# Kernel optimization log

Hardware: AMD Instinct MI355X
Metric: run time of the kernel (lower is better)

The kernel has to match this reference:

```python
import jax, jax.numpy as jnp
import numpy as np

B, N, DIN, DOUT = 8, 2048, 256, 256

def setup_inputs() -> dict:
    key = jax.random.key(0)
    k1, k2, k3 = jax.random.split(key, 3)
    H = jax.random.normal(k1, (B, N, DIN), dtype=jnp.float32)
    G = jax.random.uniform(k2, (B, N, N), dtype=jnp.float32)  # positive -> nonzero row/col sums
    # xavier_uniform-style scale for the weight
    limit = float(np.sqrt(6.0 / (DIN + DOUT)))
    W = jax.random.uniform(k3, (DIN, DOUT), dtype=jnp.float32, minval=-limit, maxval=limit)
    return {"H": H, "G": G, "W": W}

def reference(H, G, W):
    # N_e = H @ W : [b,n,dout]
    N_e = H @ W
    # symmetric part
    G_F = (G + jnp.swapaxes(G, 1, 2)) * 0.5
    # loop over k of outer products == two normalized Gram matrices:
    # G_Sin[i,j] = sum_k G[k,i]*G[k,j] / rowsum_k  == G^T diag(1/rowsum) G
    # G_So[i,j]  = sum_k G[i,k]*G[j,k] / colsum_k  == G diag(1/colsum) G^T
    rs = G.sum(axis=-1)  # [b,n] row sums
    cs = G.sum(axis=-2)  # [b,n] col sums
    G_Sin = jnp.einsum('bki,bkj->bij', G / rs[:, :, None], G)
    G_So = jnp.einsum('bik,bjk->bij', G / cs[:, None, :], G)
    H_out = jnp.concatenate([
        jax.nn.relu(G_F @ N_e),
        jax.nn.relu(G_Sin @ N_e),
        jax.nn.relu(G_So @ N_e),
    ], axis=-1)  # [b,n,3*dout]
    return H_out
```

## Files before the change

### kernel.cpp

```cpp
#include <hip/hip_runtime.h>
#include <hip/hip_bf16.h>


constexpr int NN = 2048;
constexpr long GSTR = (long)NN * NN;

using frag8   = __attribute__((ext_vector_type(8))) short;
using floatx4 = __attribute__((ext_vector_type(4))) float;
using ush8    = __attribute__((ext_vector_type(8))) unsigned short;

__device__ inline unsigned short f2bf(float x) {
    unsigned u = __float_as_uint(x);
    u += 0x7FFF + ((u >> 16) & 1);
    return (unsigned short)(u >> 16);
}
__device__ inline float bf2f(unsigned short h) {
    return __uint_as_float((unsigned)h << 16);
}
__device__ inline ushort2 pk2(float a, float b) {
    union { __hip_bfloat162 h; ushort2 u; } cv;
    cv.h = __float22bfloat162_rn(float2{a, b});
    return cv.u;
}
__device__ inline void gload_lds16(const void* g, void* l) {
    __builtin_amdgcn_global_load_lds(
        (const __attribute__((address_space(1))) void*)g,
        (__attribute__((address_space(3))) void*)l, 16, 0, 0);
}

enum { EPI_NE = 0, EPI_M1 = 1, EPI_P2 = 2, EPI_O3 = 3 };
enum { A_F32ROW = 0, A_DMA = 1 };

template <int EPI, int AMODE, int TM, int NJ>
__global__ __launch_bounds__(256) void mgemm(
    const void* __restrict__ Aptr,
    const unsigned short* __restrict__ B0,
    const unsigned short* __restrict__ B1,
    const float* __restrict__ rsraw,
    unsigned short* __restrict__ CsT,
    float* __restrict__ outp,
    const float* __restrict__ scale,
    int K, int lda, long strideA, long sB)
{
    constexpr int MF = TM / 32;
    __shared__ __align__(16) unsigned short As[TM * 64];
    __shared__ __align__(16) unsigned short Bs[64 * 64];

    const int t  = threadIdx.x;
    const int bx = blockIdx.x;
    const int xcd = bx & 7;
    const int kk  = bx >> 3;
    constexpr int PER = NJ * 8;
    const int itile = xcd + 8 * (kk / PER);
    const int rem   = kk & (PER - 1);
    const int bb    = rem / NJ;
    const int jt    = rem & (NJ - 1);
    const int i0b = itile * TM;
    const int j0  = jt * 64;

    const unsigned short* Btb =
        ((EPI == EPI_P2 && j0 >= 256) ? B1 + (long)(j0 - 256) * K
                                      : B0 + (long)j0 * K) + (long)bb * sB;

    const int w = t >> 6, l = t & 63;
    const int wm = w >> 1, wn = w & 1;
    const int quad = l >> 4, c15 = l & 15;

    const int lr  = l >> 3, ls = l & 7;

    floatx4 acc[MF][2] = {};

    for (int k0 = 0; k0 < K; k0 += 64) {
        if constexpr (AMODE == A_DMA) {
            const unsigned short* Au = (const unsigned short*)Aptr
                + (long)bb * strideA
                + (((long)itile * (K >> 7) + (k0 >> 7)) << 14);
            const int kin = k0 & 127;
            #pragma unroll
            for (int q = 0; q < TM / 32; ++q) {
                const int rt = q * 32 + w * 8;
                gload_lds16(Au + (rt + lr) * 128 + kin + ((ls ^ lr) << 3),
                            &As[rt * 64]);
            }
        } else {
            const float* Af = (const float*)Aptr + (long)bb * strideA;
            const int ar  = t >> 2;
            const int ac0 = (t & 3) * 2;
            const float* ap = Af + (long)(i0b + ar) * lda + k0 + ac0 * 8;
            const float4 x0 = *(const float4*)(ap + 0);
            const float4 x1 = *(const float4*)(ap + 4);
            const float4 x2 = *(const float4*)(ap + 8);
            const float4 x3 = *(const float4*)(ap + 12);
            union { ush8 v; ushort2 u2[4]; } p0, p1;
            p0.u2[0] = pk2(x0.x, x0.y); p0.u2[1] = pk2(x0.z, x0.w);
            p0.u2[2] = pk2(x1.x, x1.y); p0.u2[3] = pk2(x1.z, x1.w);
            p1.u2[0] = pk2(x2.x, x2.y); p1.u2[1] = pk2(x2.z, x2.w);
            p1.u2[2] = pk2(x3.x, x3.y); p1.u2[3] = pk2(x3.z, x3.w);
            const int sw = ar & 7;
            *(ush8*)&As[ar * 64 + ((ac0 ^ sw) << 3)]       = p0.v;
            *(ush8*)&As[ar * 64 + (((ac0 + 1) ^ sw) << 3)] = p1.v;
        }
        #pragma unroll
        for (int q = 0; q < 2; ++q) {
            const int rt = w * 16 + q * 8;
            gload_lds16(Btb + (long)(rt + lr) * K + k0 + ((ls ^ lr) << 3),
                        &Bs[rt * 64]);
        }
        __syncthreads();

        #pragma unroll
        for (int ks = 0; ks < 2; ++ks) {
            frag8 af[MF], bfv[2];
            const int swr = c15 & 7;
            #pragma unroll
            for (int mt = 0; mt < MF; ++mt)
                af[mt] = *(const frag8*)&As[(wm * (TM / 2) + mt * 16 + c15) * 64
                                            + (((ks * 4 + quad) ^ swr) << 3)];
            #pragma unroll
            for (int nt = 0; nt < 2; ++nt)
                bfv[nt] = *(const frag8*)&Bs[(wn * 32 + nt * 16 + c15) * 64
                                             + (((ks * 4 + quad) ^ swr) << 3)];
            #pragma unroll
            for (int mt = 0; mt < MF; ++mt)
                #pragma unroll
                for (int nt = 0; nt < 2; ++nt)
                    acc[mt][nt] = __builtin_amdgcn_mfma_f32_16x16x32_bf16(
                        af[mt], bfv[nt], acc[mt][nt], 0, 0, 0);
        }
        __syncthreads();
    }

    const long rowb = (long)bb * NN;
    #pragma unroll
    for (int mt = 0; mt < MF; ++mt) {
        const int il = wm * (TM / 2) + mt * 16 + quad * 4;
        const int ib = i0b + il;
        float4 s4 = make_float4(1.f, 1.f, 1.f, 1.f);
        if constexpr (EPI == EPI_M1) s4 = *(const float4*)(scale + rowb + ib);
        if constexpr (EPI == EPI_P2) {
            if (j0 < 256) s4 = *(const float4*)(scale + rowb + ib);
        }
        #pragma unroll
        for (int nt = 0; nt < 2; ++nt) {
            floatx4 v = acc[mt][nt];
            const int gj = j0 + wn * 32 + nt * 16 + c15;
            if constexpr (EPI == EPI_NE) {
                union { ushort4 v; ushort2 u2[2]; } p;
                p.u2[0] = pk2(v[0], v[1]); p.u2[1] = pk2(v[2], v[3]);
                *(ushort4*)(CsT + ((long)bb * 256 + gj) * 2048 + ib) = p.v;
            } else if constexpr (EPI == EPI_M1) {
                union { ushort4 v; ushort2 u2[2]; } p;
                p.u2[0] = pk2(v[0] * s4.x, v[1] * s4.y);
                p.u2[1] = pk2(v[2] * s4.z, v[3] * s4.w);
                *(ushort4*)(CsT + ((long)bb * 256 + gj) * 2048 + ib) = p.v;
            } else if constexpr (EPI == EPI_P2) {
                if (j0 < 256) {
                    union { ushort4 v; ushort2 u2[2]; } p;
                    p.u2[0] = pk2(v[0] * s4.x, v[1] * s4.y);
                    p.u2[1] = pk2(v[2] * s4.z, v[3] * s4.w);
                    *(ushort4*)(CsT + ((long)bb * 256 + gj) * 2048 + ib) = p.v;
                    const float4 rr = *(const float4*)(rsraw + rowb + ib);
                    const ushort4 m1p = *(const ushort4*)(B1 + ((long)bb * 256 + gj) * 2048 + ib);
                    const float m1v[4] = {bf2f(m1p.x) * rr.x, bf2f(m1p.y) * rr.y,
                                          bf2f(m1p.z) * rr.z, bf2f(m1p.w) * rr.w};
                    #pragma unroll
                    for (int r = 0; r < 4; ++r)
                        outp[(rowb + ib + r) * 768 + gj] = fmaxf(0.5f * (v[r] + m1v[r]), 0.f);
                } else {
                    #pragma unroll
                    for (int r = 0; r < 4; ++r)
                        outp[(rowb + ib + r) * 768 + gj] = fmaxf(v[r], 0.f);
                }
            } else {
                #pragma unroll
                for (int r = 0; r < 4; ++r)
                    outp[(rowb + ib + r) * 768 + 512 + gj] = fmaxf(v[r], 0.f);
            }
        }
    }
}

__global__ __launch_bounds__(256) void cvt_g(
    const float* __restrict__ G,
    unsigned short* __restrict__ Gbf, unsigned short* __restrict__ GbfT,
    float* __restrict__ prs, float* __restrict__ pcs)
{
    const int b  = blockIdx.z;
    const int j0 = blockIdx.x * 128, i0 = blockIdx.y * 128;
    const int t  = threadIdx.x;
    const int w  = t >> 6, l = t & 63;
    const int wm = w >> 1, wn = w & 1;
    const int rg = l >> 3, c = l & 7;

    const int ib = i0 + wm * 64 + rg * 8;
    const int jb = j0 + wn * 64 + c * 8;
    const int il = wm * 64 + rg * 8;
    const int jl = wn * 64 + c * 8;

    const long gbase = (long)b * GSTR + (((long)blockIdx.y * 16 + blockIdx.x) << 14);
    const long tbase = (long)b * GSTR + (((long)blockIdx.x * 16 + blockIdx.y) << 14);

    const float* gp = G + (long)b * GSTR + (long)ib * NN + jb;

    float4 xs[16];
    #pragma unroll
    for (int r = 0; r < 8; ++r) {
        xs[2 * r]     = *(const float4*)(gp + (long)r * NN);
        xs[2 * r + 1] = *(const float4*)(gp + (long)r * NN + 4);
    }
    __builtin_amdgcn_sched_barrier(0);

    union RowU { ush8 v; ushort2 u2[4]; unsigned u4[4]; };
    RowU rows[8];
    float csum[8] = {};
    float rsum[8];

    #pragma unroll
    for (int r = 0; r < 8; ++r) {
        const float4 x0 = xs[2 * r], x1 = xs[2 * r + 1];
        RowU rw;
        rw.u2[0] = pk2(x0.x, x0.y); rw.u2[1] = pk2(x0.z, x0.w);
        rw.u2[2] = pk2(x1.x, x1.y); rw.u2[3] = pk2(x1.z, x1.w);
        rows[r] = rw;
        *(ush8*)(Gbf + gbase + (long)(il + r) * 128 + jl) = rw.v;
        rsum[r] = x0.x + x0.y + x0.z + x0.w + x1.x + x1.y + x1.z + x1.w;
        csum[0] += x0.x; csum[1] += x0.y; csum[2] += x0.z; csum[3] += x0.w;
        csum[4] += x1.x; csum[5] += x1.y; csum[6] += x1.z; csum[7] += x1.w;
    }

    #pragma unroll
    for (int r = 0; r < 8; ++r) {
        rsum[r] += __shfl_xor(rsum[r], 1);
        rsum[r] += __shfl_xor(rsum[r], 2);
        rsum[r] += __shfl_xor(rsum[r], 4);
    }
    if (c == 0) {
        float* pp = prs + ((long)b * 32 + blockIdx.x * 2 + wn) * NN + ib;
        *(float4*)pp       = make_float4(rsum[0], rsum[1], rsum[2], rsum[3]);
        *(float4*)(pp + 4) = make_float4(rsum[4], rsum[5], rsum[6], rsum[7]);
    }

    #pragma unroll
    for (int e = 0; e < 8; ++e) {
        csum[e] += __shfl_xor(csum[e], 8);
        csum[e] += __shfl_xor(csum[e], 16);
        csum[e] += __shfl_xor(csum[e], 32);
    }
    if (rg == 0) {
        float* pp = pcs + ((long)b * 32 + blockIdx.y * 2 + wm) * NN + jb;
        *(float4*)pp       = make_float4(csum[0], csum[1], csum[2], csum[3]);
        *(float4*)(pp + 4) = make_float4(csum[4], csum[5], csum[6], csum[7]);
    }

    RowU cols[8];
    #pragma unroll
    for (int p = 0; p < 4; ++p) {
        #pragma unroll
        for (int k = 0; k < 4; ++k) {
            const unsigned a = rows[2 * p].u4[k], bq = rows[2 * p + 1].u4[k];
            cols[2 * k].u4[p]     = (a & 0xffffu) | (bq << 16);
            cols[2 * k + 1].u4[p] = (a >> 16) | (bq & 0xffff0000u);
        }
    }
    #pragma unroll
    for (int j = 0; j < 8; ++j)
        *(ush8*)(GbfT + tbase + (long)(jl + j) * 128 + il) = cols[j].v;
}

__global__ __launch_bounds__(256) void finalize(
    const float* __restrict__ prs, const float* __restrict__ pcs,
    float* __restrict__ inv_rs, float* __restrict__ rs_raw,
    float* __restrict__ inv_cs,
    const float* __restrict__ W, unsigned short* __restrict__ Wt)
{
    const int idx = blockIdx.x * 256 + threadIdx.x;
    if (blockIdx.y == 0) {
        const int b = idx >> 11, i = idx & 2047;
        float s = 0.f;
        #pragma unroll
        for (int jc = 0; jc < 32; ++jc) s += prs[((long)b * 32 + jc) * NN + i];
        inv_rs[idx] = 1.0f / s;
        rs_raw[idx] = s;
    } else if (blockIdx.y == 1) {
        const int b = idx >> 11, i = idx & 2047;
        float s = 0.f;
        #pragma unroll
        for (int ic = 0; ic < 32; ++ic) s += pcs[((long)b * 32 + ic) * NN + i];
        inv_cs[idx] = 1.0f / s;
    } else {
        #pragma unroll
        for (int e = 0; e < 4; ++e) {
            const int flat = idx * 4 + e;
            const int j = flat >> 8, k = flat & 255;
            Wt[flat] = f2bf(W[(long)k * 256 + j]);
        }
    }
}

extern "C" void kernel_launch(void* const* d_in, const int* in_sizes, int n_in,
                              void* d_out, int out_size, void* d_ws, size_t ws_size,
                              hipStream_t stream)
{
    constexpr int B = 8;
    const float* H = (const float*)d_in[0];
    const float* G = (const float*)d_in[1];
    const float* W = (const float*)d_in[2];
    float* out = (float*)d_out;

    unsigned short* ws16 = (unsigned short*)d_ws;
    unsigned short* Gbf  = ws16;
    unsigned short* GbfT = Gbf  + (long)B * GSTR;
    unsigned short* Wt   = GbfT + (long)B * GSTR;
    unsigned short* NeT  = Wt   + 65536;
    unsigned short* M1sT = NeT  + 4194304;
    unsigned short* M2sT = M1sT + 4194304;
    float* inv_rs = (float*)(M2sT + 4194304);
    float* rs_raw = inv_rs + 16384;
    float* inv_cs = rs_raw + 16384;
    float* prs    = inv_cs + 16384;
    float* pcs    = prs + (long)B * 32 * NN;

    cvt_g<<<dim3(16, 16, 8), 256, 0, stream>>>(G, Gbf, GbfT, prs, pcs);
    finalize<<<dim3(64, 3), 256, 0, stream>>>(prs, pcs, inv_rs, rs_raw, inv_cs, W, Wt);

    const long sNT = 256L * NN;
    mgemm<EPI_NE, A_F32ROW, 64, 4><<<1024, 256, 0, stream>>>(
        H, Wt, nullptr, nullptr, NeT, nullptr, nullptr,
        256, 256, 2048L * 256, 0);
    mgemm<EPI_M1, A_DMA, 128, 4><<<512, 256, 0, stream>>>(
        Gbf, NeT, nullptr, nullptr, M1sT, nullptr, inv_rs,
        2048, 2048, GSTR, sNT);
    mgemm<EPI_P2, A_DMA, 128, 8><<<1024, 256, 0, stream>>>(
        GbfT, NeT, M1sT, rs_raw, M2sT, out, inv_cs,
        2048, 2048, GSTR, sNT);
    mgemm<EPI_O3, A_DMA, 128, 4><<<512, 256, 0, stream>>>(
        Gbf, M2sT, nullptr, nullptr, nullptr, out, nullptr,
        2048, 2048, GSTR, sNT);
}
```

Baseline: 392.8 us.

## Split G conversion into streaming pass plus bf16 transpose; widen P2 N-tile

The fused fp32 G conversion/transpose kernel is split in two. A row-streaming kernel converts G to tiled bf16, computes full row sums directly and writes column partials. A second kernel then builds the transposed bf16 copy by reading the bf16 tiles rather than fp32. The mgemm template gains a WJ tile-width parameter, and the P2 GEMM uses 128-wide N tiles with half the blocks, which raises A-tile reuse and register pressure. The transpose now re-reads bf16 data in an extra launch, and the finalize step sums 128 column partials instead of 32.

```diff
diff --git a/kernel.cpp b/kernel.cpp
--- a/kernel.cpp
+++ b/kernel.cpp
@@ -31,7 +31,7 @@
 enum { EPI_NE = 0, EPI_M1 = 1, EPI_P2 = 2, EPI_O3 = 3 };
 enum { A_F32ROW = 0, A_DMA = 1 };
 
-template <int EPI, int AMODE, int TM, int NJ>
+template <int EPI, int AMODE, int TM, int WJ, int NJ>
 __global__ __launch_bounds__(256) void mgemm(
     const void* __restrict__ Aptr,
     const unsigned short* __restrict__ B0,
@@ -43,8 +43,9 @@
     int K, int lda, long strideA, long sB)
 {
     constexpr int MF = TM / 32;
+    constexpr int NF = WJ / 32;
     __shared__ __align__(16) unsigned short As[TM * 64];
-    __shared__ __align__(16) unsigned short Bs[64 * 64];
+    __shared__ __align__(16) unsigned short Bs[WJ * 64];
 
     const int t  = threadIdx.x;
     const int bx = blockIdx.x;
@@ -56,7 +57,7 @@
     const int bb    = rem / NJ;
     const int jt    = rem & (NJ - 1);
     const int i0b = itile * TM;
-    const int j0  = jt * 64;
+    const int j0  = jt * WJ;
 
     const unsigned short* Btb =
         ((EPI == EPI_P2 && j0 >= 256) ? B1 + (long)(j0 - 256) * K
@@ -68,7 +69,7 @@
 
     const int lr  = l >> 3, ls = l & 7;
 
-    floatx4 acc[MF][2] = {};
+    floatx4 acc[MF][NF] = {};
 
     for (int k0 = 0; k0 < K; k0 += 64) {
         if constexpr (AMODE == A_DMA) {
@@ -101,8 +102,8 @@
             *(ush8*)&As[ar * 64 + (((ac0 + 1) ^ sw) << 3)] = p1.v;
         }
         #pragma unroll
-        for (int q = 0; q < 2; ++q) {
-            const int rt = w * 16 + q * 8;
+        for (int q = 0; q < WJ / 32; ++q) {
+            const int rt = q * 32 + w * 8;
             gload_lds16(Btb + (long)(rt + lr) * K + k0 + ((ls ^ lr) << 3),
                         &Bs[rt * 64]);
         }
@@ -110,20 +111,20 @@
 
         #pragma unroll
         for (int ks = 0; ks < 2; ++ks) {
-            frag8 af[MF], bfv[2];
+            frag8 af[MF], bfv[NF];
             const int swr = c15 & 7;
             #pragma unroll
             for (int mt = 0; mt < MF; ++mt)
                 af[mt] = *(const frag8*)&As[(wm * (TM / 2) + mt * 16 + c15) * 64
                                             + (((ks * 4 + quad) ^ swr) << 3)];
             #pragma unroll
-            for (int nt = 0; nt < 2; ++nt)
-                bfv[nt] = *(const frag8*)&Bs[(wn * 32 + nt * 16 + c15) * 64
+            for (int nt = 0; nt < NF; ++nt)
+                bfv[nt] = *(const frag8*)&Bs[(wn * (WJ / 2) + nt * 16 + c15) * 64
                                              + (((ks * 4 + quad) ^ swr) << 3)];
             #pragma unroll
             for (int mt = 0; mt < MF; ++mt)
                 #pragma unroll
-                for (int nt = 0; nt < 2; ++nt)
+                for (int nt = 0; nt < NF; ++nt)
                     acc[mt][nt] = __builtin_amdgcn_mfma_f32_16x16x32_bf16(
                         af[mt], bfv[nt], acc[mt][nt], 0, 0, 0);
         }
@@ -141,9 +142,9 @@
             if (j0 < 256) s4 = *(const float4*)(scale + rowb + ib);
         }
         #pragma unroll
-        for (int nt = 0; nt < 2; ++nt) {
+        for (int nt = 0; nt < NF; ++nt) {
             floatx4 v = acc[mt][nt];
-            const int gj = j0 + wn * 32 + nt * 16 + c15;
+            const int gj = j0 + wn * (WJ / 2) + nt * 16 + c15;
             if constexpr (EPI == EPI_NE) {
                 union { ushort4 v; ushort2 u2[2]; } p;
                 p.u2[0] = pk2(v[0], v[1]); p.u2[1] = pk2(v[2], v[3]);
@@ -180,79 +181,87 @@
     }
 }
 
-__global__ __launch_bounds__(256) void cvt_g(
+__global__ __launch_bounds__(256) void cvt_stream(
     const float* __restrict__ G,
-    unsigned short* __restrict__ Gbf, unsigned short* __restrict__ GbfT,
-    float* __restrict__ prs, float* __restrict__ pcs)
+    unsigned short* __restrict__ Gbf,
+    float* __restrict__ pcs,
+    float* __restrict__ inv_rs, float* __restrict__ rs_raw)
+{
+    __shared__ float sm[4][16];
+    const int b  = blockIdx.y;
+    const int s  = blockIdx.x;
+    const int i0 = s * 16;
+    const int t  = threadIdx.x;
+    const int c8 = t * 8;
+    const int w  = t >> 6, l = t & 63;
+
+    const float* gp = G + (long)b * GSTR + (long)i0 * NN + c8;
+    unsigned short* gb = Gbf + (long)b * GSTR;
+    const int tc = c8 >> 7, cin = c8 & 127;
+
+    float csum[8] = {};
+    float rp[16];
+
+    #pragma unroll
+    for (int r = 0; r < 16; ++r) {
+        const float4 x0 = *(const float4*)(gp + (long)r * NN);
+        const float4 x1 = *(const float4*)(gp + (long)r * NN + 4);
+        union { ush8 v; ushort2 u2[4]; } pk;
+        pk.u2[0] = pk2(x0.x, x0.y); pk.u2[1] = pk2(x0.z, x0.w);
+        pk.u2[2] = pk2(x1.x, x1.y); pk.u2[3] = pk2(x1.z, x1.w);
+        const int gi = i0 + r;
+        *(ush8*)(gb + (((long)(gi >> 7) * 16 + tc) << 14) + ((gi & 127) << 7) + cin) = pk.v;
+        rp[r] = x0.x + x0.y + x0.z + x0.w + x1.x + x1.y + x1.z + x1.w;
+        csum[0] += x0.x; csum[1] += x0.y; csum[2] += x0.z; csum[3] += x0.w;
+        csum[4] += x1.x; csum[5] += x1.y; csum[6] += x1.z; csum[7] += x1.w;
+    }
+
+    float* pp = pcs + ((long)b * 128 + s) * NN + c8;
+    *(float4*)pp       = make_float4(csum[0], csum[1], csum[2], csum[3]);
+    *(float4*)(pp + 4) = make_float4(csum[4], csum[5], csum[6], csum[7]);
+
+    #pragma unroll
+    for (int r = 0; r < 16; ++r) {
+        rp[r] += __shfl_xor(rp[r], 1);
+        rp[r] += __shfl_xor(rp[r], 2);
+        rp[r] += __shfl_xor(rp[r], 4);
+        rp[r] += __shfl_xor(rp[r], 8);
+        rp[r] += __shfl_xor(rp[r], 16);
+        rp[r] += __shfl_xor(rp[r], 32);
+    }
+    if (l == 0) {
+        #pragma unroll
+        for (int r = 0; r < 16; ++r) sm[w][r] = rp[r];
+    }
+    __syncthreads();
+    if (t < 16) {
+        const float s_ = sm[0][t] + sm[1][t] + sm[2][t] + sm[3][t];
+        rs_raw[(long)b * NN + i0 + t] = s_;
+        inv_rs[(long)b * NN + i0 + t] = 1.0f / s_;
+    }
+}
+
+__global__ __launch_bounds__(256) void cvt_t(
+    const unsigned short* __restrict__ Gbf, unsigned short* __restrict__ GbfT)
 {
     const int b  = blockIdx.z;
-    const int j0 = blockIdx.x * 128, i0 = blockIdx.y * 128;
-    const int t  = threadIdx.x;
-    const int w  = t >> 6, l = t & 63;
+    const int tr = blockIdx.y, tc = blockIdx.x;
+    const long src = (long)b * GSTR + (((long)tr * 16 + tc) << 14);
+    const long dst = (long)b * GSTR + (((long)tc * 16 + tr) << 14);
+    const int t = threadIdx.x;
+    const int w = t >> 6, l = t & 63;
     const int wm = w >> 1, wn = w & 1;
     const int rg = l >> 3, c = l & 7;
-
-    const int ib = i0 + wm * 64 + rg * 8;
-    const int jb = j0 + wn * 64 + c * 8;
     const int il = wm * 64 + rg * 8;
     const int jl = wn * 64 + c * 8;
 
-    const long gbase = (long)b * GSTR + (((long)blockIdx.y * 16 + blockIdx.x) << 14);
-    const long tbase = (long)b * GSTR + (((long)blockIdx.x * 16 + blockIdx.y) << 14);
-
-    const float* gp = G + (long)b * GSTR + (long)ib * NN + jb;
-
-    float4 xs[16];
-    #pragma unroll
-    for (int r = 0; r < 8; ++r) {
-        xs[2 * r]     = *(const float4*)(gp + (long)r * NN);
-        xs[2 * r + 1] = *(const float4*)(gp + (long)r * NN + 4);
-    }
+    union RowU { ush8 v; unsigned u4[4]; };
+    RowU rows[8], cols[8];
+    #pragma unroll
+    for (int r = 0; r < 8; ++r)
+        rows[r].v = *(const ush8*)(Gbf + src + (long)(il + r) * 128 + jl);
     __builtin_amdgcn_sched_barrier(0);
 
-    union RowU { ush8 v; ushort2 u2[4]; unsigned u4[4]; };
-    RowU rows[8];
-    float csum[8] = {};
-    float rsum[8];
-
-    #pragma unroll
-    for (int r = 0; r < 8; ++r) {
-        const float4 x0 = xs[2 * r], x1 = xs[2 * r + 1];
-        RowU rw;
-        rw.u2[0] = pk2(x0.x, x0.y); rw.u2[1] = pk2(x0.z, x0.w);
-        rw.u2[2] = pk2(x1.x, x1.y); rw.u2[3] = pk2(x1.z, x1.w);
-        rows[r] = rw;
-        *(ush8*)(Gbf + gbase + (long)(il + r) * 128 + jl) = rw.v;
-        rsum[r] = x0.x + x0.y + x0.z + x0.w + x1.x + x1.y + x1.z + x1.w;
-        csum[0] += x0.x; csum[1] += x0.y; csum[2] += x0.z; csum[3] += x0.w;
-        csum[4] += x1.x; csum[5] += x1.y; csum[6] += x1.z; csum[7] += x1.w;
-    }
-
-    #pragma unroll
-    for (int r = 0; r < 8; ++r) {
-        rsum[r] += __shfl_xor(rsum[r], 1);
-        rsum[r] += __shfl_xor(rsum[r], 2);
-        rsum[r] += __shfl_xor(rsum[r], 4);
-    }
-    if (c == 0) {
-        float* pp = prs + ((long)b * 32 + blockIdx.x * 2 + wn) * NN + ib;
-        *(float4*)pp       = make_float4(rsum[0], rsum[1], rsum[2], rsum[3]);
-        *(float4*)(pp + 4) = make_float4(rsum[4], rsum[5], rsum[6], rsum[7]);
-    }
-
-    #pragma unroll
-    for (int e = 0; e < 8; ++e) {
-        csum[e] += __shfl_xor(csum[e], 8);
-        csum[e] += __shfl_xor(csum[e], 16);
-        csum[e] += __shfl_xor(csum[e], 32);
-    }
-    if (rg == 0) {
-        float* pp = pcs + ((long)b * 32 + blockIdx.y * 2 + wm) * NN + jb;
-        *(float4*)pp       = make_float4(csum[0], csum[1], csum[2], csum[3]);
-        *(float4*)(pp + 4) = make_float4(csum[4], csum[5], csum[6], csum[7]);
-    }
-
-    RowU cols[8];
     #pragma unroll
     for (int p = 0; p < 4; ++p) {
         #pragma unroll
@@ -264,12 +273,11 @@
     }
     #pragma unroll
     for (int j = 0; j < 8; ++j)
-        *(ush8*)(GbfT + tbase + (long)(jl + j) * 128 + il) = cols[j].v;
+        *(ush8*)(GbfT + dst + (long)(jl + j) * 128 + il) = cols[j].v;
 }
 
 __global__ __launch_bounds__(256) void finalize(
-    const float* __restrict__ prs, const float* __restrict__ pcs,
-    float* __restrict__ inv_rs, float* __restrict__ rs_raw,
+    const float* __restrict__ pcs,
     float* __restrict__ inv_cs,
     const float* __restrict__ W, unsigned short* __restrict__ Wt)
 {
@@ -277,15 +285,7 @@
     if (blockIdx.y == 0) {
         const int b = idx >> 11, i = idx & 2047;
         float s = 0.f;
-        #pragma unroll
-        for (int jc = 0; jc < 32; ++jc) s += prs[((long)b * 32 + jc) * NN + i];
-        inv_rs[idx] = 1.0f / s;
-        rs_raw[idx] = s;
-    } else if (blockIdx.y == 1) {
-        const int b = idx >> 11, i = idx & 2047;
-        float s = 0.f;
-        #pragma unroll
-        for (int ic = 0; ic < 32; ++ic) s += pcs[((long)b * 32 + ic) * NN + i];
+        for (int ic = 0; ic < 128; ++ic) s += pcs[((long)b * 128 + ic) * NN + i];
         inv_cs[idx] = 1.0f / s;
     } else {
         #pragma unroll
@@ -317,23 +317,23 @@
     float* inv_rs = (float*)(M2sT + 4194304);
     float* rs_raw = inv_rs + 16384;
     float* inv_cs = rs_raw + 16384;
-    float* prs    = inv_cs + 16384;
-    float* pcs    = prs + (long)B * 32 * NN;
-
-    cvt_g<<<dim3(16, 16, 8), 256, 0, stream>>>(G, Gbf, GbfT, prs, pcs);
-    finalize<<<dim3(64, 3), 256, 0, stream>>>(prs, pcs, inv_rs, rs_raw, inv_cs, W, Wt);
+    float* pcs    = inv_cs + 16384;
+
+    cvt_stream<<<dim3(128, 8), 256, 0, stream>>>(G, Gbf, pcs, inv_rs, rs_raw);
+    cvt_t<<<dim3(16, 16, 8), 256, 0, stream>>>(Gbf, GbfT);
+    finalize<<<dim3(64, 2), 256, 0, stream>>>(pcs, inv_cs, W, Wt);
 
     const long sNT = 256L * NN;
-    mgemm<EPI_NE, A_F32ROW, 64, 4><<<1024, 256, 0, stream>>>(
+    mgemm<EPI_NE, A_F32ROW, 64, 64, 4><<<1024, 256, 0, stream>>>(
         H, Wt, nullptr, nullptr, NeT, nullptr, nullptr,
         256, 256, 2048L * 256, 0);
-    mgemm<EPI_M1, A_DMA, 128, 4><<<512, 256, 0, stream>>>(
+    mgemm<EPI_M1, A_DMA, 128, 64, 4><<<512, 256, 0, stream>>>(
         Gbf, NeT, nullptr, nullptr, M1sT, nullptr, inv_rs,
         2048, 2048, GSTR, sNT);
-    mgemm<EPI_P2, A_DMA, 128, 8><<<1024, 256, 0, stream>>>(
+    mgemm<EPI_P2, A_DMA, 128, 128, 4><<<512, 256, 0, stream>>>(
         GbfT, NeT, M1sT, rs_raw, M2sT, out, inv_cs,
         2048, 2048, GSTR, sNT);
-    mgemm<EPI_O3, A_DMA, 128, 4><<<512, 256, 0, stream>>>(
+    mgemm<EPI_O3, A_DMA, 128, 64, 4><<<512, 256, 0, stream>>>(
         Gbf, M2sT, nullptr, nullptr, nullptr, out, nullptr,
         2048, 2048, GSTR, sNT);
 }
```

Result: faster. 374.9 us (-4.6%).
